# Performance work log

Measured on AMD Instinct MI355X. Metric: run time of the kernel, lower is better.

The kernel has to match this reference:

```python
import jax, jax.numpy as jnp
import numpy as np
import math

D_MODEL = 96
D_STATE = 16
D_CONV = 3
EXPAND = 2
D_INNER = EXPAND * D_MODEL          # 192
DT_RANK = math.ceil(D_MODEL / 16)   # 6
B_SZ, H_SZ, W_SZ = 2, 56, 56


def setup_inputs() -> dict:
    key = jax.random.key(0)
    ks = jax.random.split(key, 10)
    x = jax.random.normal(ks[0], (B_SZ, H_SZ, W_SZ, D_MODEL), jnp.float32)
    W_in = jax.random.normal(ks[1], (D_MODEL, 2 * D_INNER), jnp.float32) * 0.02
    conv_w = jax.random.normal(ks[2], (D_CONV, D_CONV, 1, D_INNER), jnp.float32) * 0.1
    conv_b = jax.random.normal(ks[3], (D_INNER,), jnp.float32) * 0.02
    W_xproj = jax.random.normal(ks[4], (D_INNER, DT_RANK + 2 * D_STATE), jnp.float32) * 0.02
    dt_std = DT_RANK ** -0.5
    W_dt = jax.random.uniform(ks[5], (DT_RANK, D_INNER), jnp.float32, -dt_std, dt_std)
    # dt_proj bias init: inverse-softplus of dt ~ LogUniform(dt_min, dt_max)
    dt_min, dt_max = 1e-3, 1e-1
    dt = jnp.exp(jax.random.uniform(ks[6], (D_INNER,), jnp.float32)
                 * (math.log(dt_max) - math.log(dt_min)) + math.log(dt_min))
    dt = jnp.clip(dt, 1e-4, None)
    b_dt = dt + jnp.log(-jnp.expm1(-dt))
    # A_log initialized to broadcast arange(1..d_state) (as in the source, no log taken)
    A_log = jnp.tile(jnp.arange(1, D_STATE + 1, dtype=jnp.float32)[None, :], (D_INNER, 1))
    D_skip = jnp.ones((D_INNER,), jnp.float32)
    W_out = jax.random.normal(ks[7], (D_INNER, D_MODEL), jnp.float32) * 0.02
    return {"x": x, "W_in": W_in, "conv_w": conv_w, "conv_b": conv_b,
            "W_xproj": W_xproj, "W_dt": W_dt, "b_dt": b_dt,
            "A_log": A_log, "D_skip": D_skip, "W_out": W_out}


def _selective_scan(xs, dt, A, Bm, Cm, D_skip):
    """Canonical Mamba selective scan.
    xs, dt: (G, L, C); Bm, Cm: (G, L, N); A: (C, N); D_skip: (C,).
    h_l = exp(dt_l * A) * h_{l-1} + dt_l * B_l * x_l ;  y_l = <h_l, C_l> + D * x_l
    """
    dA = jnp.exp(dt[..., None] * A)                              # (G,L,C,N)
    dBx = dt[..., None] * Bm[:, :, None, :] * xs[..., None]      # (G,L,C,N)

    def step(h, inp):
        dA_l, dBx_l, C_l = inp                                   # (G,C,N),(G,C,N),(G,N)
        h = dA_l * h + dBx_l
        y = jnp.einsum('gcn,gn->gc', h, C_l)
        return h, y

    G, L, C = xs.shape
    h0 = jnp.zeros((G, C, D_STATE), xs.dtype)
    _, ys = jax.lax.scan(step, h0, (jnp.moveaxis(dA, 1, 0),
                                    jnp.moveaxis(dBx, 1, 0),
                                    jnp.moveaxis(Cm, 1, 0)))
    ys = jnp.moveaxis(ys, 0, 1)                                  # (G,L,C)
    return ys + D_skip * xs


def reference(x, W_in, conv_w, conv_b, W_xproj, W_dt, b_dt, A_log, D_skip, W_out):
    B, H, W, _ = x.shape  # H == W required (source sums transposed scans directly)
    xz = x @ W_in                                                # (B,H,W,2*d_inner)
    xm, z = jnp.split(xz, 2, axis=-1)
    pad = (D_CONV - 1) // 2
    xm = jax.lax.conv_general_dilated(
        xm, conv_w, (1, 1), [(pad, pad), (pad, pad)],
        dimension_numbers=('NHWC', 'HWIO', 'NHWC'),
        feature_group_count=D_INNER) + conv_b                    # depthwise conv
    # 4 scan directions
    xt = jnp.swapaxes(xm, 1, 2)
    xs4 = jnp.stack([xm, jnp.flip(xm, 2), xt, jnp.flip(xt, 1)], 0)  # (4,B,H,W,C)
    G, L = 4 * B, H * W
    xs = xs4.reshape(G, L, D_INNER)
    x_dbl = xs @ W_xproj                                          # (G,L,dt_rank+2N)
    dtr, Bm, Cm = jnp.split(x_dbl, [DT_RANK, DT_RANK + D_STATE], axis=-1)
    dt = jax.nn.softplus(dtr @ W_dt + b_dt)                       # (G,L,d_inner)
    A = -jnp.exp(A_log)                                           # (d_inner, N)
    ys = _selective_scan(xs, dt, A, Bm, Cm, D_skip)               # (G,L,d_inner)
    y = ys.reshape(4, B, H, W, D_INNER).sum(0)                    # sum 4 directions
    y = jax.nn.silu(z) * y
    return y @ W_out                                              # (B,H,W,d_model)
```

## Files before the change

### kernel.cpp

```cpp
#include <hip/hip_runtime.h>
#include <math.h>

#define NPIX 6272
#define LVAL 3136
#define CIN 192
#define NST 16
#define HW 56

__device__ __forceinline__ float softplusf(float v) {
    return (v > 20.0f) ? v : log1pf(expf(v));
}

__device__ __forceinline__ void dir_geom(int d, int b, int& si, int& sj, int& off) {
    if (d == 0)      { si = HW;  sj = 1;   off = b * LVAL; }
    else if (d == 1) { si = HW;  sj = -1;  off = b * LVAL + (HW - 1); }
    else if (d == 2) { si = 1;   sj = HW;  off = b * LVAL; }
    else             { si = -1;  sj = HW;  off = b * LVAL + (HW - 1); }
}

__global__ __launch_bounds__(384) void k_inproj(
    const float* __restrict__ x, const float* __restrict__ W_in,
    float* __restrict__ xm, float* __restrict__ z)
{
    __shared__ __align__(16) float xs[96][20];
    const int p0 = blockIdx.x * 16;
    const int t = threadIdx.x;
    for (int e = t; e < 16 * 96; e += 384) {
        int p = e / 96, kk = e % 96;
        xs[kk][p] = x[p0 * 96 + e];
    }
    __syncthreads();
    float acc[16];
#pragma unroll
    for (int p = 0; p < 16; ++p) acc[p] = 0.f;
    for (int k = 0; k < 96; ++k) {
        float w = W_in[k * 384 + t];
        float4 x0 = *(const float4*)&xs[k][0];
        float4 x1 = *(const float4*)&xs[k][4];
        float4 x2 = *(const float4*)&xs[k][8];
        float4 x3 = *(const float4*)&xs[k][12];
        acc[0]  = fmaf(x0.x, w, acc[0]);  acc[1]  = fmaf(x0.y, w, acc[1]);
        acc[2]  = fmaf(x0.z, w, acc[2]);  acc[3]  = fmaf(x0.w, w, acc[3]);
        acc[4]  = fmaf(x1.x, w, acc[4]);  acc[5]  = fmaf(x1.y, w, acc[5]);
        acc[6]  = fmaf(x1.z, w, acc[6]);  acc[7]  = fmaf(x1.w, w, acc[7]);
        acc[8]  = fmaf(x2.x, w, acc[8]);  acc[9]  = fmaf(x2.y, w, acc[9]);
        acc[10] = fmaf(x2.z, w, acc[10]); acc[11] = fmaf(x2.w, w, acc[11]);
        acc[12] = fmaf(x3.x, w, acc[12]); acc[13] = fmaf(x3.y, w, acc[13]);
        acc[14] = fmaf(x3.z, w, acc[14]); acc[15] = fmaf(x3.w, w, acc[15]);
    }
#pragma unroll
    for (int p = 0; p < 16; ++p) {
        int pix = p0 + p;
        if (t < 192) xm[pix * CIN + t] = acc[p];
        else         z[pix * CIN + (t - 192)] = acc[p];
    }
}

__global__ __launch_bounds__(256) void k_conv(
    const float* __restrict__ xm, const float* __restrict__ cw,
    const float* __restrict__ cb, float* __restrict__ xcv)
{
    int e = blockIdx.x * 256 + threadIdx.x;
    if (e >= NPIX * (CIN / 4)) return;
    int cq = (e % (CIN / 4)) * 4;
    int pix = e / (CIN / 4);
    int w = pix % HW;
    int rest = pix / HW;
    int h = rest % HW;
    int b = rest / HW;
    float4 acc = *(const float4*)&cb[cq];
#pragma unroll
    for (int ky = 0; ky < 3; ++ky) {
        int hh = h + ky - 1;
        if (hh < 0 || hh >= HW) continue;
#pragma unroll
        for (int kx = 0; kx < 3; ++kx) {
            int ww = w + kx - 1;
            if (ww < 0 || ww >= HW) continue;
            float4 xv = *(const float4*)&xm[((b * HW + hh) * HW + ww) * CIN + cq];
            float4 wv = *(const float4*)&cw[(ky * 3 + kx) * CIN + cq];
            acc.x = fmaf(xv.x, wv.x, acc.x);
            acc.y = fmaf(xv.y, wv.y, acc.y);
            acc.z = fmaf(xv.z, wv.z, acc.z);
            acc.w = fmaf(xv.w, wv.w, acc.w);
        }
    }
    *(float4*)&xcv[pix * CIN + cq] = acc;
}

__global__ __launch_bounds__(512) void k_xproj_dt(
    const float* __restrict__ xcv, const float* __restrict__ W_xproj,
    const float* __restrict__ W_dt, const float* __restrict__ b_dt,
    float* __restrict__ Bp, float* __restrict__ Cp, float2* __restrict__ dtx2)
{
    __shared__ __align__(16) float xs[192][28];
    __shared__ float part[2][24][40];
    __shared__ float dtr_lds[24][8];
    const int p0 = blockIdx.x * 24;
    const int t = threadIdx.x;
    for (int e = t; e < 24 * 192; e += 512) {
        int p = e / 192, kk = e % 192;
        int pix = p0 + p;
        xs[kk][p] = (pix < NPIX) ? xcv[pix * CIN + kk] : 0.f;
    }
    __syncthreads();
    const int th = t & 255;
    const int kh = t >> 8;
    const int j  = th % 40;
    const int pq = th / 40;
    if (pq < 6) {
        const int jc = (j < 38) ? j : 37;
        float a0 = 0.f, a1 = 0.f, a2 = 0.f, a3 = 0.f;
        const int k0 = kh * 96;
        for (int k = k0; k < k0 + 96; ++k) {
            float w = W_xproj[k * 38 + jc];
            float4 xv = *(const float4*)&xs[k][pq * 4];
            a0 = fmaf(xv.x, w, a0); a1 = fmaf(xv.y, w, a1);
            a2 = fmaf(xv.z, w, a2); a3 = fmaf(xv.w, w, a3);
        }
        part[kh][pq * 4 + 0][j] = a0;
        part[kh][pq * 4 + 1][j] = a1;
        part[kh][pq * 4 + 2][j] = a2;
        part[kh][pq * 4 + 3][j] = a3;
    }
    __syncthreads();
    if (kh == 0 && pq < 6 && j < 38) {
#pragma unroll
        for (int q = 0; q < 4; ++q) {
            int p = pq * 4 + q;
            float r = part[0][p][j] + part[1][p][j];
            int pix = p0 + p;
            if (j < 6) dtr_lds[p][j] = r;
            if (pix < NPIX) {
                if (j < 6)       ;
                else if (j < 22) Bp[pix * NST + (j - 6)] = r;
                else             Cp[pix * NST + (j - 22)] = r;
            }
        }
    }
    __syncthreads();
    for (int e = t; e < 24 * 192; e += 512) {
        int p = e / 192, c = e % 192;
        int pix = p0 + p;
        if (pix >= NPIX) continue;
        float v = b_dt[c];
#pragma unroll
        for (int r = 0; r < 6; ++r)
            v = fmaf(dtr_lds[p][r], W_dt[r * CIN + c], v);
        dtx2[(size_t)pix * CIN + c] = make_float2(softplusf(v), xs[c][p]);
    }
}

template<int CHUNK>
__global__ __launch_bounds__(384) void k_scan_p1(
    const float2* __restrict__ dtx2, const float* __restrict__ Bp,
    const float* __restrict__ A_log,
    float* __restrict__ Pbuf, float* __restrict__ qbuf)
{
    static_assert(CHUNK % 4 == 0, "CHUNK must be multiple of 4");
    constexpr int CPR = HW / CHUNK;
    __shared__ __align__(16) float Bs[CHUNK * NST];
    const int g = blockIdx.y;
    const int k = blockIdx.x;
    const int t = threadIdx.x;
    const int wv = t >> 6;
    const int lane = t & 63;
    const int cl = lane & 31, nh = lane >> 5;
    const int c = wv * 32 + cl;
    const int n0 = nh * 8;
    const int d = g >> 1, b = g & 1;
    int si, sj, off;
    dir_geom(d, b, si, sj, off);
    const int base = off + (k / CPR) * si + ((k % CPR) * CHUNK) * sj;

    for (int e = t; e < CHUNK * NST; e += 384) {
        int jj = e >> 4, n = e & 15;
        Bs[e] = Bp[(base + jj * sj) * NST + n];
    }

    const float LOG2E = 1.4426950408889634f;
    float a2[8];
    {
        const float4* Ar = (const float4*)(A_log + c * NST + n0);
#pragma unroll
        for (int q = 0; q < 2; ++q) {
            float4 v = Ar[q];
            a2[q*4+0] = -expf(v.x) * LOG2E;
            a2[q*4+1] = -expf(v.y) * LOG2E;
            a2[q*4+2] = -expf(v.z) * LOG2E;
            a2[q*4+3] = -expf(v.w) * LOG2E;
        }
    }
    __syncthreads();

    float h[8];
#pragma unroll
    for (int i = 0; i < 8; ++i) h[i] = 0.f;
    float Sdt = 0.f;

    const float2* dp = dtx2 + (size_t)base * CIN + c;
    const ptrdiff_t dstep = (ptrdiff_t)sj * CIN;

#define P1_STEP(DVV, JJ) do {                                            \
        float dt_c = (DVV).x, x_c = (DVV).y;                             \
        float dtx = dt_c * x_c;                                          \
        Sdt += dt_c;                                                     \
        const float4* Brow = (const float4*)(Bs + (JJ) * NST + n0);      \
        float4 t0 = Brow[0], t1 = Brow[1];                               \
        float Bv[8] = {t0.x,t0.y,t0.z,t0.w,t1.x,t1.y,t1.z,t1.w};         \
        _Pragma("unroll")                                                \
        for (int i = 0; i < 8; ++i) {                                    \
            float dA = exp2f(dt_c * a2[i]);                              \
            h[i] = fmaf(dA, h[i], dtx * Bv[i]);                          \
        }                                                                \
    } while (0)

    float2 v0 = dp[0];
    float2 v1 = dp[dstep];
    float2 v2 = dp[2 * dstep];
    float2 v3 = dp[3 * dstep];
    for (int jj = 0; jj < CHUNK; jj += 4) {
        const int j4 = (jj + 4 < CHUNK) ? jj + 4 : CHUNK - 4;
        float2 nv0 = dp[(ptrdiff_t)(j4 + 0) * dstep];
        float2 nv1 = dp[(ptrdiff_t)(j4 + 1) * dstep];
        float2 nv2 = dp[(ptrdiff_t)(j4 + 2) * dstep];
        float2 nv3 = dp[(ptrdiff_t)(j4 + 3) * dstep];
        P1_STEP(v0, jj + 0);
        P1_STEP(v1, jj + 1);
        P1_STEP(v2, jj + 2);
        P1_STEP(v3, jj + 3);
        v0 = nv0; v1 = nv1; v2 = nv2; v3 = nv3;
    }
#undef P1_STEP

    float P[8];
#pragma unroll
    for (int i = 0; i < 8; ++i) P[i] = exp2f(a2[i] * Sdt);

    float4* Pd = (float4*)(Pbuf + ((size_t)(k * 8 + g) * CIN + c) * NST + n0);
    float4* qd = (float4*)(qbuf + ((size_t)(k * 8 + g) * CIN + c) * NST + n0);
    Pd[0] = make_float4(P[0], P[1], P[2], P[3]);
    Pd[1] = make_float4(P[4], P[5], P[6], P[7]);
    qd[0] = make_float4(h[0], h[1], h[2], h[3]);
    qd[1] = make_float4(h[4], h[5], h[6], h[7]);
}

__global__ __launch_bounds__(256) void k_scan_fix(
    const float* __restrict__ Pbuf, float* __restrict__ qbuf, int nch)
{
    const int g = blockIdx.y;
    const int lo = blockIdx.x * 256 + threadIdx.x;
    const size_t stride = (size_t)8 * CIN * NST;
    size_t idx  = (size_t)g * CIN * NST + lo;
    size_t pidx = idx;
    float Pr[8], qr[8];
#pragma unroll
    for (int i = 0; i < 8; ++i) { Pr[i] = Pbuf[pidx]; qr[i] = qbuf[pidx]; pidx += stride; }
    float h = 0.f;
    for (int k = 0; k < nch; k += 8) {
        float Pn[8], qn[8];
        if (k + 8 < nch) {
#pragma unroll
            for (int i = 0; i < 8; ++i) {
                Pn[i] = Pbuf[pidx + (size_t)i * stride];
                qn[i] = qbuf[pidx + (size_t)i * stride];
            }
        } else {
#pragma unroll
            for (int i = 0; i < 8; ++i) { Pn[i] = 0.f; qn[i] = 0.f; }
        }
#pragma unroll
        for (int i = 0; i < 8; ++i) {
            qbuf[idx] = h;
            h = fmaf(Pr[i], h, qr[i]);
            idx += stride;
        }
#pragma unroll
        for (int i = 0; i < 8; ++i) { Pr[i] = Pn[i]; qr[i] = qn[i]; }
        pidx += (size_t)8 * stride;
    }
}

template<int CHUNK>
__global__ __launch_bounds__(384) void k_scan_p2(
    const float2* __restrict__ dtx2, const float* __restrict__ Bp,
    const float* __restrict__ Cp, const float* __restrict__ A_log,
    const float* __restrict__ D_skip,
    const float* __restrict__ qbuf, float* __restrict__ Y4)
{
    static_assert(CHUNK % 4 == 0, "CHUNK must be multiple of 4");
    constexpr int CPR = HW / CHUNK;
    __shared__ __align__(16) float Bs[CHUNK * NST];
    __shared__ __align__(16) float Cs[CHUNK * NST];
    const int g = blockIdx.y;
    const int k = blockIdx.x;
    const int t = threadIdx.x;
    const int wv = t >> 6;
    const int lane = t & 63;
    const int cl = lane & 31, nh = lane >> 5;
    const int c = wv * 32 + cl;
    const int n0 = nh * 8;
    const int d = g >> 1, b = g & 1;
    int si, sj, off;
    dir_geom(d, b, si, sj, off);
    const int base = off + (k / CPR) * si + ((k % CPR) * CHUNK) * sj;

    for (int e = t; e < CHUNK * NST; e += 384) {
        int jj = e >> 4, n = e & 15;
        int pa = (base + jj * sj) * NST + n;
        Bs[e] = Bp[pa];
        Cs[e] = Cp[pa];
    }

    const float LOG2E = 1.4426950408889634f;
    float a2[8];
    {
        const float4* Ar = (const float4*)(A_log + c * NST + n0);
#pragma unroll
        for (int q = 0; q < 2; ++q) {
            float4 v = Ar[q];
            a2[q*4+0] = -expf(v.x) * LOG2E;
            a2[q*4+1] = -expf(v.y) * LOG2E;
            a2[q*4+2] = -expf(v.z) * LOG2E;
            a2[q*4+3] = -expf(v.w) * LOG2E;
        }
    }
    const float Dc = D_skip[c];

    float h[8];
    {
        const float4* qd = (const float4*)(qbuf + ((size_t)(k * 8 + g) * CIN + c) * NST + n0);
        float4 v0q = qd[0], v1q = qd[1];
        h[0]=v0q.x; h[1]=v0q.y; h[2]=v0q.z; h[3]=v0q.w;
        h[4]=v1q.x; h[5]=v1q.y; h[6]=v1q.z; h[7]=v1q.w;
    }
    __syncthreads();

    float* yo = Y4 + ((size_t)d * NPIX + (size_t)b * LVAL + (size_t)k * CHUNK) * CIN;

    const float2* dp = dtx2 + (size_t)base * CIN + c;
    const ptrdiff_t dstep = (ptrdiff_t)sj * CIN;

#define P2_STEP(DVV, JJ) do {                                            \
        float dt_c = (DVV).x, x_c = (DVV).y;                             \
        float dtx = dt_c * x_c;                                          \
        const float4* Brow = (const float4*)(Bs + (JJ) * NST + n0);      \
        const float4* Crow = (const float4*)(Cs + (JJ) * NST + n0);      \
        float4 t0 = Brow[0], t1 = Brow[1];                               \
        float4 u0 = Crow[0], u1 = Crow[1];                               \
        float Bv[8] = {t0.x,t0.y,t0.z,t0.w,t1.x,t1.y,t1.z,t1.w};         \
        float Cv[8] = {u0.x,u0.y,u0.z,u0.w,u1.x,u1.y,u1.z,u1.w};         \
        float yc0 = 0.f, yc1 = 0.f;                                      \
        _Pragma("unroll")                                                \
        for (int i = 0; i < 8; i += 2) {                                 \
            float dA0 = exp2f(dt_c * a2[i]);                             \
            float dA1 = exp2f(dt_c * a2[i+1]);                           \
            h[i]   = fmaf(dA0, h[i],   dtx * Bv[i]);                     \
            h[i+1] = fmaf(dA1, h[i+1], dtx * Bv[i+1]);                   \
            yc0 = fmaf(h[i],   Cv[i],   yc0);                            \
            yc1 = fmaf(h[i+1], Cv[i+1], yc1);                            \
        }                                                                \
        float yc = yc0 + yc1;                                            \
        yc += __shfl_xor(yc, 32, 64);                                    \
        if (nh == 0)                                                     \
            yo[(JJ) * CIN + c] = fmaf(Dc, x_c, yc);                      \
    } while (0)

    float2 v0 = dp[0];
    float2 v1 = dp[dstep];
    float2 v2 = dp[2 * dstep];
    float2 v3 = dp[3 * dstep];
    for (int jj = 0; jj < CHUNK; jj += 4) {
        const int j4 = (jj + 4 < CHUNK) ? jj + 4 : CHUNK - 4;
        float2 nv0 = dp[(ptrdiff_t)(j4 + 0) * dstep];
        float2 nv1 = dp[(ptrdiff_t)(j4 + 1) * dstep];
        float2 nv2 = dp[(ptrdiff_t)(j4 + 2) * dstep];
        float2 nv3 = dp[(ptrdiff_t)(j4 + 3) * dstep];
        P2_STEP(v0, jj + 0);
        P2_STEP(v1, jj + 1);
        P2_STEP(v2, jj + 2);
        P2_STEP(v3, jj + 3);
        v0 = nv0; v1 = nv1; v2 = nv2; v3 = nv3;
    }
#undef P2_STEP
}

__global__ __launch_bounds__(384) void k_gateout(
    const float* __restrict__ Y4, const float* __restrict__ z,
    const float* __restrict__ W_out, float* __restrict__ out)
{
    __shared__ __align__(16) float xs[192][20];
    const int p0 = blockIdx.x * 16;
    const int t = threadIdx.x;
    const size_t NP = (size_t)NPIX * CIN;
    for (int e = t; e < 16 * 192; e += 384) {
        int p = e / 192, c = e % 192;
        size_t idx = (size_t)(p0 + p) * CIN + c;
        float s = Y4[idx] + Y4[idx + NP] + Y4[idx + 2 * NP] + Y4[idx + 3 * NP];
        float zz = z[idx];
        float sig = 1.f / (1.f + expf(-zz));
        xs[c][p] = zz * sig * s;
    }
    __syncthreads();
    const int j  = t % 96;
    const int ph = t / 96;
    float acc[4] = {0.f, 0.f, 0.f, 0.f};
    for (int k = 0; k < 192; ++k) {
        float w = W_out[k * 96 + j];
        float4 xv = *(const float4*)&xs[k][ph * 4];
        acc[0] = fmaf(xv.x, w, acc[0]); acc[1] = fmaf(xv.y, w, acc[1]);
        acc[2] = fmaf(xv.z, w, acc[2]); acc[3] = fmaf(xv.w, w, acc[3]);
    }
#pragma unroll
    for (int p = 0; p < 4; ++p)
        out[(p0 + ph * 4 + p) * 96 + j] = acc[p];
}

template<int CHUNK>
static void launch_scan(const float2* dtx2, const float* Bp, const float* Cp,
                        const float* A_log, const float* D_skip,
                        float* Pbuf, float* qbuf, float* Y4, hipStream_t stream)
{
    const int nch = LVAL / CHUNK;
    k_scan_p1<CHUNK><<<dim3(nch, 8), 384, 0, stream>>>(dtx2, Bp, A_log, Pbuf, qbuf);
    k_scan_fix<<<dim3(12, 8), 256, 0, stream>>>(Pbuf, qbuf, nch);
    k_scan_p2<CHUNK><<<dim3(nch, 8), 384, 0, stream>>>(dtx2, Bp, Cp, A_log, D_skip, qbuf, Y4);
}

extern "C" void kernel_launch(void* const* d_in, const int* in_sizes, int n_in,
                              void* d_out, int out_size, void* d_ws, size_t ws_size,
                              hipStream_t stream) {
    const float* x      = (const float*)d_in[0];
    const float* W_in   = (const float*)d_in[1];
    const float* conv_w = (const float*)d_in[2];
    const float* conv_b = (const float*)d_in[3];
    const float* W_xproj= (const float*)d_in[4];
    const float* W_dt   = (const float*)d_in[5];
    const float* b_dt   = (const float*)d_in[6];
    const float* A_log  = (const float*)d_in[7];
    const float* D_skip = (const float*)d_in[8];
    const float* W_out  = (const float*)d_in[9];
    float* out = (float*)d_out;

    float* ws   = (float*)d_ws;
    float* xm   = ws;
    float* z    = xm  + NPIX * CIN;
    float* xcv  = z   + NPIX * CIN;
    float2* dtx2= (float2*)(xcv + NPIX * CIN);
    float* Bp   = (float*)(dtx2 + (size_t)NPIX * CIN);
    float* Cp   = Bp  + NPIX * NST;
    float* Y4   = Cp  + NPIX * NST;
    float* Pbuf = Y4  + (size_t)4 * NPIX * CIN;

    const size_t base_fl = 11038720;
    const size_t ws_fl = ws_size / 4;
    int chunk;
    if (ws_fl >= base_fl + (size_t)2 * 112 * 24576) chunk = 28;
    else                                            chunk = 56;
    float* qbuf = Pbuf + (size_t)(LVAL / chunk) * 8 * CIN * NST;

    k_inproj  <<<NPIX / 16, 384, 0, stream>>>(x, W_in, xm, z);
    k_conv    <<<(NPIX * (CIN / 4)) / 256, 256, 0, stream>>>(xm, conv_w, conv_b, xcv);
    k_xproj_dt<<<(NPIX + 23) / 24, 512, 0, stream>>>(xcv, W_xproj, W_dt, b_dt, Bp, Cp, dtx2);
    if (chunk == 28) launch_scan<28>(dtx2, Bp, Cp, A_log, D_skip, Pbuf, qbuf, Y4, stream);
    else             launch_scan<56>(dtx2, Bp, Cp, A_log, D_skip, Pbuf, qbuf, Y4, stream);
    k_gateout <<<NPIX / 16, 384, 0, stream>>>(Y4, z, W_out, out);
}
```

Baseline: 196.0 us.

## Split scan state dimension four ways per channel and double scan grid

New measurement: 195.6 us. No clear change (-0.2%).

```diff
diff --git a/kernel.cpp b/kernel.cpp
--- a/kernel.cpp
+++ b/kernel.cpp
@@ -162,12 +162,13 @@
     __shared__ __align__(16) float Bs[CHUNK * NST];
     const int g = blockIdx.y;
     const int k = blockIdx.x;
+    const int ch = blockIdx.z;
     const int t = threadIdx.x;
     const int wv = t >> 6;
     const int lane = t & 63;
-    const int cl = lane & 31, nh = lane >> 5;
-    const int c = wv * 32 + cl;
-    const int n0 = nh * 8;
+    const int cl = lane & 15, nh = lane >> 4;
+    const int c = ch * 96 + wv * 16 + cl;
+    const int n0 = nh * 4;
     const int d = g >> 1, b = g & 1;
     int si, sj, off;
     dir_geom(d, b, si, sj, off);
@@ -179,23 +180,19 @@
     }
 
     const float LOG2E = 1.4426950408889634f;
-    float a2[8];
+    float a2[4];
     {
-        const float4* Ar = (const float4*)(A_log + c * NST + n0);
-#pragma unroll
-        for (int q = 0; q < 2; ++q) {
-            float4 v = Ar[q];
-            a2[q*4+0] = -expf(v.x) * LOG2E;
-            a2[q*4+1] = -expf(v.y) * LOG2E;
-            a2[q*4+2] = -expf(v.z) * LOG2E;
-            a2[q*4+3] = -expf(v.w) * LOG2E;
-        }
-    }
-    __syncthreads();
-
-    float h[8];
-#pragma unroll
-    for (int i = 0; i < 8; ++i) h[i] = 0.f;
+        float4 v = *(const float4*)(A_log + c * NST + n0);
+        a2[0] = -expf(v.x) * LOG2E;
+        a2[1] = -expf(v.y) * LOG2E;
+        a2[2] = -expf(v.z) * LOG2E;
+        a2[3] = -expf(v.w) * LOG2E;
+    }
+    __syncthreads();
+
+    float h[4];
+#pragma unroll
+    for (int i = 0; i < 4; ++i) h[i] = 0.f;
     float Sdt = 0.f;
 
     const float2* dp = dtx2 + (size_t)base * CIN + c;
@@ -205,11 +202,10 @@
         float dt_c = (DVV).x, x_c = (DVV).y;                             \
         float dtx = dt_c * x_c;                                          \
         Sdt += dt_c;                                                     \
-        const float4* Brow = (const float4*)(Bs + (JJ) * NST + n0);      \
-        float4 t0 = Brow[0], t1 = Brow[1];                               \
-        float Bv[8] = {t0.x,t0.y,t0.z,t0.w,t1.x,t1.y,t1.z,t1.w};         \
+        float4 t0 = *(const float4*)(Bs + (JJ) * NST + n0);              \
+        float Bv[4] = {t0.x, t0.y, t0.z, t0.w};                          \
         _Pragma("unroll")                                                \
-        for (int i = 0; i < 8; ++i) {                                    \
+        for (int i = 0; i < 4; ++i) {                                    \
             float dA = exp2f(dt_c * a2[i]);                              \
             h[i] = fmaf(dA, h[i], dtx * Bv[i]);                          \
         }                                                                \
@@ -233,16 +229,14 @@
     }
 #undef P1_STEP
 
-    float P[8];
-#pragma unroll
-    for (int i = 0; i < 8; ++i) P[i] = exp2f(a2[i] * Sdt);
+    float P[4];
+#pragma unroll
+    for (int i = 0; i < 4; ++i) P[i] = exp2f(a2[i] * Sdt);
 
     float4* Pd = (float4*)(Pbuf + ((size_t)(k * 8 + g) * CIN + c) * NST + n0);
     float4* qd = (float4*)(qbuf + ((size_t)(k * 8 + g) * CIN + c) * NST + n0);
     Pd[0] = make_float4(P[0], P[1], P[2], P[3]);
-    Pd[1] = make_float4(P[4], P[5], P[6], P[7]);
     qd[0] = make_float4(h[0], h[1], h[2], h[3]);
-    qd[1] = make_float4(h[4], h[5], h[6], h[7]);
 }
 
 __global__ __launch_bounds__(256) void k_scan_fix(
@@ -294,12 +288,13 @@
     __shared__ __align__(16) float Cs[CHUNK * NST];
     const int g = blockIdx.y;
     const int k = blockIdx.x;
+    const int ch = blockIdx.z;
     const int t = threadIdx.x;
     const int wv = t >> 6;
     const int lane = t & 63;
-    const int cl = lane & 31, nh = lane >> 5;
-    const int c = wv * 32 + cl;
-    const int n0 = nh * 8;
+    const int cl = lane & 15, nh = lane >> 4;
+    const int c = ch * 96 + wv * 16 + cl;
+    const int n0 = nh * 4;
     const int d = g >> 1, b = g & 1;
     int si, sj, off;
     dir_geom(d, b, si, sj, off);
@@ -313,26 +308,20 @@
     }
 
     const float LOG2E = 1.4426950408889634f;
-    float a2[8];
+    float a2[4];
     {
-        const float4* Ar = (const float4*)(A_log + c * NST + n0);
-#pragma unroll
-        for (int q = 0; q < 2; ++q) {
-            float4 v = Ar[q];
-            a2[q*4+0] = -expf(v.x) * LOG2E;
-            a2[q*4+1] = -expf(v.y) * LOG2E;
-            a2[q*4+2] = -expf(v.z) * LOG2E;
-            a2[q*4+3] = -expf(v.w) * LOG2E;
-        }
+        float4 v = *(const float4*)(A_log + c * NST + n0);
+        a2[0] = -expf(v.x) * LOG2E;
+        a2[1] = -expf(v.y) * LOG2E;
+        a2[2] = -expf(v.z) * LOG2E;
+        a2[3] = -expf(v.w) * LOG2E;
     }
     const float Dc = D_skip[c];
 
-    float h[8];
+    float h[4];
     {
-        const float4* qd = (const float4*)(qbuf + ((size_t)(k * 8 + g) * CIN + c) * NST + n0);
-        float4 v0q = qd[0], v1q = qd[1];
+        float4 v0q = *(const float4*)(qbuf + ((size_t)(k * 8 + g) * CIN + c) * NST + n0);
         h[0]=v0q.x; h[1]=v0q.y; h[2]=v0q.z; h[3]=v0q.w;
-        h[4]=v1q.x; h[5]=v1q.y; h[6]=v1q.z; h[7]=v1q.w;
     }
     __syncthreads();
 
@@ -344,15 +333,13 @@
 #define P2_STEP(DVV, JJ) do {                                            \
         float dt_c = (DVV).x, x_c = (DVV).y;                             \
         float dtx = dt_c * x_c;                                          \
-        const float4* Brow = (const float4*)(Bs + (JJ) * NST + n0);      \
-        const float4* Crow = (const float4*)(Cs + (JJ) * NST + n0);      \
-        float4 t0 = Brow[0], t1 = Brow[1];                               \
-        float4 u0 = Crow[0], u1 = Crow[1];                               \
-        float Bv[8] = {t0.x,t0.y,t0.z,t0.w,t1.x,t1.y,t1.z,t1.w};         \
-        float Cv[8] = {u0.x,u0.y,u0.z,u0.w,u1.x,u1.y,u1.z,u1.w};         \
+        float4 t0 = *(const float4*)(Bs + (JJ) * NST + n0);              \
+        float4 u0 = *(const float4*)(Cs + (JJ) * NST + n0);              \
+        float Bv[4] = {t0.x, t0.y, t0.z, t0.w};                          \
+        float Cv[4] = {u0.x, u0.y, u0.z, u0.w};                          \
         float yc0 = 0.f, yc1 = 0.f;                                      \
         _Pragma("unroll")                                                \
-        for (int i = 0; i < 8; i += 2) {                                 \
+        for (int i = 0; i < 4; i += 2) {                                 \
             float dA0 = exp2f(dt_c * a2[i]);                             \
             float dA1 = exp2f(dt_c * a2[i+1]);                           \
             h[i]   = fmaf(dA0, h[i],   dtx * Bv[i]);                     \
@@ -361,6 +348,7 @@
             yc1 = fmaf(h[i+1], Cv[i+1], yc1);                            \
         }                                                                \
         float yc = yc0 + yc1;                                            \
+        yc += __shfl_xor(yc, 16, 64);                                    \
         yc += __shfl_xor(yc, 32, 64);                                    \
         if (nh == 0)                                                     \
             yo[(JJ) * CIN + c] = fmaf(Dc, x_c, yc);                      \
@@ -422,9 +410,9 @@
                         float* Pbuf, float* qbuf, float* Y4, hipStream_t stream)
 {
     const int nch = LVAL / CHUNK;
-    k_scan_p1<CHUNK><<<dim3(nch, 8), 384, 0, stream>>>(dtx2, Bp, A_log, Pbuf, qbuf);
+    k_scan_p1<CHUNK><<<dim3(nch, 8, 2), 384, 0, stream>>>(dtx2, Bp, A_log, Pbuf, qbuf);
     k_scan_fix<<<dim3(12, 8), 256, 0, stream>>>(Pbuf, qbuf, nch);
-    k_scan_p2<CHUNK><<<dim3(nch, 8), 384, 0, stream>>>(dtx2, Bp, Cp, A_log, D_skip, qbuf, Y4);
+    k_scan_p2<CHUNK><<<dim3(nch, 8, 2), 384, 0, stream>>>(dtx2, Bp, Cp, A_log, D_skip, qbuf, Y4);
 }
 
 extern "C" void kernel_launch(void* const* d_in, const int* in_sizes, int n_in,
```
